# Kernel tuning notes

Hardware: AMD Instinct MI355X
Metric: run time of the kernel (lower is better)

## Reference

```python
import jax, jax.numpy as jnp
import numpy as np

B, A, N, E, H, OUT = 32, 16, 10000, 256, 256, 2

def setup_inputs() -> dict:
    key = jax.random.key(0)
    k1, k2, k3, k4, k5, k6 = jax.random.split(key, 6)
    abs_actions = jax.random.normal(k1, (B, A), dtype=jnp.float32)
    assignments = jax.random.randint(k2, (B, N), 0, A, dtype=jnp.int64)
    emb = jax.random.normal(k3, (N, E), dtype=jnp.float32)  # ground_agent_embedding.weight
    s1 = 1.0 / np.sqrt(1 + E)
    W1 = jax.random.uniform(k4, (1 + E, H), jnp.float32, -s1, s1)
    b1 = jnp.zeros((H,), jnp.float32)
    s2 = 1.0 / np.sqrt(H)
    W2 = jax.random.uniform(k5, (H, OUT), jnp.float32, -s2, s2)
    b2 = jnp.zeros((OUT,), jnp.float32)
    return {"abs_actions": abs_actions, "abstract_agent_assignments": assignments,
            "emb": emb, "W1": W1, "b1": b1, "W2": W2, "b2": b2}

def reference(abs_actions, abstract_agent_assignments, emb, W1, b1, W2, b2):
    # per-batch gather: assigned[b, n] = abs_actions[b, assignments[b, n]]  -> (B, N)
    assigned = jnp.take_along_axis(abs_actions, abstract_agent_assignments, axis=1)
    # concat scalar action with broadcast embedding table -> (B, N, 1+E)
    x = jnp.concatenate(
        [assigned[..., None], jnp.broadcast_to(emb[None], (assigned.shape[0],) + emb.shape)],
        axis=-1)
    # shared small MLP (MultiChannelNet, n_channels=1): Linear -> ReLU -> Linear
    h = jax.nn.relu(jnp.einsum("bnf,fh->bnh", x, W1) + b1)
    return jnp.einsum("bnh,ho->bno", h, W2) + b2  # (B, N, OUT) action logits
```

## Files before the change

### kernel.cpp

```cpp
#include <hip/hip_runtime.h>


constexpr int B_ = 32, A_ = 16, N_ = 10000, E_ = 256, H_ = 256;
constexpr int TN   = 40;
constexpr int NBLK = N_ / TN;

__global__ __launch_bounds__(256, 1) void decoder_fused(
    const float* __restrict__ abs_actions,
    const int*   __restrict__ asgn,
    const float* __restrict__ emb,
    const float* __restrict__ W1,
    const float* __restrict__ b1,
    const float* __restrict__ W2,
    const float* __restrict__ b2,
    float* __restrict__ out)
{
    __shared__ float u[TN * 260];
    __shared__ float vals[B_ * 41];
    __shared__ float w1r[H_];
    __shared__ float w2s[2 * H_];

    const int t  = threadIdx.x;
    const int n0 = blockIdx.x * TN;

    {
        const float4* src = reinterpret_cast<const float4*>(emb + (size_t)n0 * E_);
        float4* dst = reinterpret_cast<float4*>(u);
        #pragma unroll
        for (int q = 0; q < 10; ++q) dst[t + 256 * q] = src[t + 256 * q];
    }
    w1r[t]       = W1[t];
    w2s[t]       = W2[t];
    w2s[256 + t] = W2[256 + t];
    #pragma unroll
    for (int q = 0; q < 5; ++q) {
        int p = t + 256 * q;
        int b = p / 40, n = p - b * 40;
        int a = asgn[b * N_ + n0 + n];
        vals[b * 41 + n] = abs_actions[b * A_ + a];
    }
    __syncthreads();

    const int hq = t & 63;
    const int h0 = hq * 4;
    const int ng = t >> 6;
    const int nb = ng * 10;

    float acc[10][4];
    {
        const float4 bv = *reinterpret_cast<const float4*>(b1 + h0);
        #pragma unroll
        for (int i = 0; i < 10; ++i) {
            acc[i][0] = bv.x; acc[i][1] = bv.y; acc[i][2] = bv.z; acc[i][3] = bv.w;
        }
    }

    const float* pw = W1 + E_ + h0;
    float4 wa = *reinterpret_cast<const float4*>(pw + 0 * 256);
    float4 wb = *reinterpret_cast<const float4*>(pw + 1 * 256);
    float4 wc = *reinterpret_cast<const float4*>(pw + 2 * 256);
    float4 wd = *reinterpret_cast<const float4*>(pw + 3 * 256);

    for (int k = 0; k < 256; k += 4) {
        const int kn = (k + 4) & 255;
        float4 na_ = *reinterpret_cast<const float4*>(pw + (kn + 0) * 256);
        float4 nb_ = *reinterpret_cast<const float4*>(pw + (kn + 1) * 256);
        float4 nc_ = *reinterpret_cast<const float4*>(pw + (kn + 2) * 256);
        float4 nd_ = *reinterpret_cast<const float4*>(pw + (kn + 3) * 256);
        #pragma unroll
        for (int i = 0; i < 10; ++i) {
            const float4 e = *reinterpret_cast<const float4*>(&u[(nb + i) * 256 + k]);
            acc[i][0] = fmaf(e.x, wa.x, acc[i][0]);
            acc[i][0] = fmaf(e.y, wb.x, acc[i][0]);
            acc[i][0] = fmaf(e.z, wc.x, acc[i][0]);
            acc[i][0] = fmaf(e.w, wd.x, acc[i][0]);
            acc[i][1] = fmaf(e.x, wa.y, acc[i][1]);
            acc[i][1] = fmaf(e.y, wb.y, acc[i][1]);
            acc[i][1] = fmaf(e.z, wc.y, acc[i][1]);
            acc[i][1] = fmaf(e.w, wd.y, acc[i][1]);
            acc[i][2] = fmaf(e.x, wa.z, acc[i][2]);
            acc[i][2] = fmaf(e.y, wb.z, acc[i][2]);
            acc[i][2] = fmaf(e.z, wc.z, acc[i][2]);
            acc[i][2] = fmaf(e.w, wd.z, acc[i][2]);
            acc[i][3] = fmaf(e.x, wa.w, acc[i][3]);
            acc[i][3] = fmaf(e.y, wb.w, acc[i][3]);
            acc[i][3] = fmaf(e.z, wc.w, acc[i][3]);
            acc[i][3] = fmaf(e.w, wd.w, acc[i][3]);
        }
        wa = na_; wb = nb_; wc = nc_; wd = nd_;
    }

    __syncthreads();
    #pragma unroll
    for (int i = 0; i < 10; ++i) {
        float4 v; v.x = acc[i][0]; v.y = acc[i][1]; v.z = acc[i][2]; v.w = acc[i][3];
        *reinterpret_cast<float4*>(&u[(nb + i) * 260 + h0]) = v;
    }
    __syncthreads();

    const float2 b2v = *reinterpret_cast<const float2*>(b2);
    float oacc[5][2];
    int   pn[5], pb[5];
    float pv[5];
    #pragma unroll
    for (int q = 0; q < 5; ++q) {
        int p = t + 256 * q;
        int b = p / 40, n = p - b * 40;
        pb[q] = b; pn[q] = n;
        pv[q] = vals[b * 41 + n];
        oacc[q][0] = 0.f; oacc[q][1] = 0.f;
    }

    #pragma unroll 2
    for (int h = 0; h < 256; h += 4) {
        const float4 wv = *reinterpret_cast<const float4*>(&w1r[h]);
        const float4 p0 = *reinterpret_cast<const float4*>(&w2s[2 * h]);
        const float4 p1 = *reinterpret_cast<const float4*>(&w2s[2 * h + 4]);
        #pragma unroll
        for (int q = 0; q < 5; ++q) {
            const float4 c = *reinterpret_cast<const float4*>(&u[pn[q] * 260 + h]);
            const float v = pv[q];
            float t0 = fmaxf(fmaf(v, wv.x, c.x), 0.f);
            float t1 = fmaxf(fmaf(v, wv.y, c.y), 0.f);
            float t2 = fmaxf(fmaf(v, wv.z, c.z), 0.f);
            float t3 = fmaxf(fmaf(v, wv.w, c.w), 0.f);
            oacc[q][0] = fmaf(t0, p0.x, oacc[q][0]);
            oacc[q][1] = fmaf(t0, p0.y, oacc[q][1]);
            oacc[q][0] = fmaf(t1, p0.z, oacc[q][0]);
            oacc[q][1] = fmaf(t1, p0.w, oacc[q][1]);
            oacc[q][0] = fmaf(t2, p1.x, oacc[q][0]);
            oacc[q][1] = fmaf(t2, p1.y, oacc[q][1]);
            oacc[q][0] = fmaf(t3, p1.z, oacc[q][0]);
            oacc[q][1] = fmaf(t3, p1.w, oacc[q][1]);
        }
    }

    #pragma unroll
    for (int q = 0; q < 5; ++q) {
        float2 o; o.x = oacc[q][0] + b2v.x; o.y = oacc[q][1] + b2v.y;
        *reinterpret_cast<float2*>(out + ((size_t)pb[q] * N_ + n0 + pn[q]) * 2) = o;
    }
}

extern "C" void kernel_launch(void* const* d_in, const int* in_sizes, int n_in,
                              void* d_out, int out_size, void* d_ws, size_t ws_size,
                              hipStream_t stream) {
    const float* abs_actions = (const float*)d_in[0];
    const int*   asgn        = (const int*)d_in[1];
    const float* emb         = (const float*)d_in[2];
    const float* W1          = (const float*)d_in[3];
    const float* b1          = (const float*)d_in[4];
    const float* W2          = (const float*)d_in[5];
    const float* b2          = (const float*)d_in[6];
    float*       out         = (float*)d_out;

    decoder_fused<<<NBLK, 256, 0, stream>>>(abs_actions, asgn, emb, W1, b1, W2, b2, out);
}
```

Before: 35.68 us.

## Compute embedding projection with bf16 MFMA using pre-transposed W1

Adds a prep kernel that transposes the embedding rows of W1 and converts them to bf16 in a global buffer. The main kernel converts embedding tiles to bf16 in shared memory and computes the N×E by E×H projection with 16x16x32 bf16 MFMA instructions instead of scalar FP32 FMAs. The tile shrinks to 16 nodes per block with two blocks per CU. This cuts FP32 ALU work on the dominant GEMM, at the cost of bf16 rounding error and an extra kernel launch per call.

```diff
diff --git a/kernel.cpp b/kernel.cpp
--- a/kernel.cpp
+++ b/kernel.cpp
@@ -2,10 +2,33 @@
 
 
 constexpr int B_ = 32, A_ = 16, N_ = 10000, E_ = 256, H_ = 256;
-constexpr int TN   = 40;
-constexpr int NBLK = N_ / TN;
+constexpr int TN = 16, NBLK = N_ / TN;
 
-__global__ __launch_bounds__(256, 1) void decoder_fused(
+typedef __attribute__((ext_vector_type(8))) short bf16x8;
+typedef __attribute__((ext_vector_type(4))) float f32x4;
+
+__device__ __align__(16) ushort g_w1t[H_ * E_];
+
+static __device__ __forceinline__ ushort f2bf(float x) {
+    union { float f; unsigned u; } c; c.f = x;
+    unsigned r = c.u + 0x7fff + ((c.u >> 16) & 1);
+    return (ushort)(r >> 16);
+}
+
+__global__ __launch_bounds__(256, 1) void prep_w1t_k(const float* __restrict__ W1) {
+    __shared__ float tile[64][65];
+    const int bk = blockIdx.x >> 2, bh = blockIdx.x & 3;
+    const int tx = threadIdx.x & 63, ty = threadIdx.x >> 6;
+    #pragma unroll
+    for (int kk = ty; kk < 64; kk += 4)
+        tile[kk][tx] = W1[(size_t)(1 + bk * 64 + kk) * H_ + bh * 64 + tx];
+    __syncthreads();
+    #pragma unroll
+    for (int hh = ty; hh < 64; hh += 4)
+        g_w1t[(size_t)(bh * 64 + hh) * E_ + bk * 64 + tx] = f2bf(tile[tx][hh]);
+}
+
+__global__ __launch_bounds__(256, 2) void decoder_main(
     const float* __restrict__ abs_actions,
     const int*   __restrict__ asgn,
     const float* __restrict__ emb,
@@ -15,130 +38,108 @@
     const float* __restrict__ b2,
     float* __restrict__ out)
 {
-    __shared__ float u[TN * 260];
-    __shared__ float vals[B_ * 41];
-    __shared__ float w1r[H_];
-    __shared__ float w2s[2 * H_];
+    __shared__ ushort eb[TN * 264];
+    __shared__ float  u[TN * 260];
+    __shared__ float  vals[B_ * 17];
+    __shared__ float  w1r[H_];
+    __shared__ float  w2s[2 * H_];
 
     const int t  = threadIdx.x;
     const int n0 = blockIdx.x * TN;
 
+    #pragma unroll
+    for (int q = 0; q < 2; ++q) {
+        const int p = t + 256 * q, b = p >> 4, n = p & 15;
+        vals[b * 17 + n] = abs_actions[b * A_ + asgn[(size_t)b * N_ + n0 + n]];
+    }
+
     {
-        const float4* src = reinterpret_cast<const float4*>(emb + (size_t)n0 * E_);
-        float4* dst = reinterpret_cast<float4*>(u);
+        const int row = t >> 4, col = (t & 15) << 4;
+        const float4* src = reinterpret_cast<const float4*>(emb + (size_t)(n0 + row) * E_ + col);
+        const float4 q0 = src[0], q1 = src[1], q2 = src[2], q3 = src[3];
+        union { ushort us[16]; bf16x8 v[2]; } pk;
+        const float f[16] = {q0.x,q0.y,q0.z,q0.w, q1.x,q1.y,q1.z,q1.w,
+                             q2.x,q2.y,q2.z,q2.w, q3.x,q3.y,q3.z,q3.w};
         #pragma unroll
-        for (int q = 0; q < 10; ++q) dst[t + 256 * q] = src[t + 256 * q];
+        for (int i = 0; i < 16; ++i) pk.us[i] = f2bf(f[i]);
+        bf16x8* dst = reinterpret_cast<bf16x8*>(&eb[row * 264 + col]);
+        dst[0] = pk.v[0]; dst[1] = pk.v[1];
     }
     w1r[t]       = W1[t];
     w2s[t]       = W2[t];
     w2s[256 + t] = W2[256 + t];
-    #pragma unroll
-    for (int q = 0; q < 5; ++q) {
-        int p = t + 256 * q;
-        int b = p / 40, n = p - b * 40;
-        int a = asgn[b * N_ + n0 + n];
-        vals[b * 41 + n] = abs_actions[b * A_ + a];
+    __syncthreads();
+
+    {
+        const int lane = t & 63, w = t >> 6;
+        const int lr = lane & 15;
+        const int lk = (lane >> 4) << 3;
+        f32x4 acc[4];
+        #pragma unroll
+        for (int ct = 0; ct < 4; ++ct) {
+            const float bv = b1[w * 64 + ct * 16 + lr];
+            acc[ct] = (f32x4){bv, bv, bv, bv};
+        }
+        #pragma unroll
+        for (int ks = 0; ks < 8; ++ks) {
+            const bf16x8 af = *reinterpret_cast<const bf16x8*>(&eb[lr * 264 + ks * 32 + lk]);
+            #pragma unroll
+            for (int ct = 0; ct < 4; ++ct) {
+                const bf16x8 bfv = *reinterpret_cast<const bf16x8*>(
+                    &g_w1t[(size_t)(w * 64 + ct * 16 + lr) * E_ + ks * 32 + lk]);
+                acc[ct] = __builtin_amdgcn_mfma_f32_16x16x32_bf16(af, bfv, acc[ct], 0, 0, 0);
+            }
+        }
+        #pragma unroll
+        for (int ct = 0; ct < 4; ++ct)
+            #pragma unroll
+            for (int r = 0; r < 4; ++r)
+                u[((lane >> 4) * 4 + r) * 260 + w * 64 + ct * 16 + lr] = acc[ct][r];
     }
     __syncthreads();
 
-    const int hq = t & 63;
-    const int h0 = hq * 4;
-    const int ng = t >> 6;
-    const int nb = ng * 10;
+    {
+        const float2 b2v = { b2[0], b2[1] };
+        float oacc[2][2];
+        int   pnn[2], pbb[2];
+        float pv[2];
+        #pragma unroll
+        for (int q = 0; q < 2; ++q) {
+            const int p = t + 256 * q, b = p >> 4, n = p & 15;
+            pbb[q] = b; pnn[q] = n;
+            pv[q] = vals[b * 17 + n];
+            oacc[q][0] = 0.f; oacc[q][1] = 0.f;
+        }
 
-    float acc[10][4];
-    {
-        const float4 bv = *reinterpret_cast<const float4*>(b1 + h0);
+        #pragma unroll 2
+        for (int h = 0; h < 256; h += 4) {
+            const float4 wv = *reinterpret_cast<const float4*>(&w1r[h]);
+            const float4 p0 = *reinterpret_cast<const float4*>(&w2s[2 * h]);
+            const float4 p1 = *reinterpret_cast<const float4*>(&w2s[2 * h + 4]);
+            #pragma unroll
+            for (int q = 0; q < 2; ++q) {
+                const float4 c = *reinterpret_cast<const float4*>(&u[pnn[q] * 260 + h]);
+                const float v = pv[q];
+                const float t0 = fmaxf(fmaf(v, wv.x, c.x), 0.f);
+                const float t1 = fmaxf(fmaf(v, wv.y, c.y), 0.f);
+                const float t2 = fmaxf(fmaf(v, wv.z, c.z), 0.f);
+                const float t3 = fmaxf(fmaf(v, wv.w, c.w), 0.f);
+                oacc[q][0] = fmaf(t0, p0.x, oacc[q][0]);
+                oacc[q][1] = fmaf(t0, p0.y, oacc[q][1]);
+                oacc[q][0] = fmaf(t1, p0.z, oacc[q][0]);
+                oacc[q][1] = fmaf(t1, p0.w, oacc[q][1]);
+                oacc[q][0] = fmaf(t2, p1.x, oacc[q][0]);
+                oacc[q][1] = fmaf(t2, p1.y, oacc[q][1]);
+                oacc[q][0] = fmaf(t3, p1.z, oacc[q][0]);
+                oacc[q][1] = fmaf(t3, p1.w, oacc[q][1]);
+            }
+        }
+
         #pragma unroll
-        for (int i = 0; i < 10; ++i) {
-            acc[i][0] = bv.x; acc[i][1] = bv.y; acc[i][2] = bv.z; acc[i][3] = bv.w;
+        for (int q = 0; q < 2; ++q) {
+            float2 o; o.x = oacc[q][0] + b2v.x; o.y = oacc[q][1] + b2v.y;
+            *reinterpret_cast<float2*>(out + ((size_t)pbb[q] * N_ + n0 + pnn[q]) * 2) = o;
         }
-    }
-
-    const float* pw = W1 + E_ + h0;
-    float4 wa = *reinterpret_cast<const float4*>(pw + 0 * 256);
-    float4 wb = *reinterpret_cast<const float4*>(pw + 1 * 256);
-    float4 wc = *reinterpret_cast<const float4*>(pw + 2 * 256);
-    float4 wd = *reinterpret_cast<const float4*>(pw + 3 * 256);
-
-    for (int k = 0; k < 256; k += 4) {
-        const int kn = (k + 4) & 255;
-        float4 na_ = *reinterpret_cast<const float4*>(pw + (kn + 0) * 256);
-        float4 nb_ = *reinterpret_cast<const float4*>(pw + (kn + 1) * 256);
-        float4 nc_ = *reinterpret_cast<const float4*>(pw + (kn + 2) * 256);
-        float4 nd_ = *reinterpret_cast<const float4*>(pw + (kn + 3) * 256);
-        #pragma unroll
-        for (int i = 0; i < 10; ++i) {
-            const float4 e = *reinterpret_cast<const float4*>(&u[(nb + i) * 256 + k]);
-            acc[i][0] = fmaf(e.x, wa.x, acc[i][0]);
-            acc[i][0] = fmaf(e.y, wb.x, acc[i][0]);
-            acc[i][0] = fmaf(e.z, wc.x, acc[i][0]);
-            acc[i][0] = fmaf(e.w, wd.x, acc[i][0]);
-            acc[i][1] = fmaf(e.x, wa.y, acc[i][1]);
-            acc[i][1] = fmaf(e.y, wb.y, acc[i][1]);
-            acc[i][1] = fmaf(e.z, wc.y, acc[i][1]);
-            acc[i][1] = fmaf(e.w, wd.y, acc[i][1]);
-            acc[i][2] = fmaf(e.x, wa.z, acc[i][2]);
-            acc[i][2] = fmaf(e.y, wb.z, acc[i][2]);
-            acc[i][2] = fmaf(e.z, wc.z, acc[i][2]);
-            acc[i][2] = fmaf(e.w, wd.z, acc[i][2]);
-            acc[i][3] = fmaf(e.x, wa.w, acc[i][3]);
-            acc[i][3] = fmaf(e.y, wb.w, acc[i][3]);
-            acc[i][3] = fmaf(e.z, wc.w, acc[i][3]);
-            acc[i][3] = fmaf(e.w, wd.w, acc[i][3]);
-        }
-        wa = na_; wb = nb_; wc = nc_; wd = nd_;
-    }
-
-    __syncthreads();
-    #pragma unroll
-    for (int i = 0; i < 10; ++i) {
-        float4 v; v.x = acc[i][0]; v.y = acc[i][1]; v.z = acc[i][2]; v.w = acc[i][3];
-        *reinterpret_cast<float4*>(&u[(nb + i) * 260 + h0]) = v;
-    }
-    __syncthreads();
-
-    const float2 b2v = *reinterpret_cast<const float2*>(b2);
-    float oacc[5][2];
-    int   pn[5], pb[5];
-    float pv[5];
-    #pragma unroll
-    for (int q = 0; q < 5; ++q) {
-        int p = t + 256 * q;
-        int b = p / 40, n = p - b * 40;
-        pb[q] = b; pn[q] = n;
-        pv[q] = vals[b * 41 + n];
-        oacc[q][0] = 0.f; oacc[q][1] = 0.f;
-    }
-
-    #pragma unroll 2
-    for (int h = 0; h < 256; h += 4) {
-        const float4 wv = *reinterpret_cast<const float4*>(&w1r[h]);
-        const float4 p0 = *reinterpret_cast<const float4*>(&w2s[2 * h]);
-        const float4 p1 = *reinterpret_cast<const float4*>(&w2s[2 * h + 4]);
-        #pragma unroll
-        for (int q = 0; q < 5; ++q) {
-            const float4 c = *reinterpret_cast<const float4*>(&u[pn[q] * 260 + h]);
-            const float v = pv[q];
-            float t0 = fmaxf(fmaf(v, wv.x, c.x), 0.f);
-            float t1 = fmaxf(fmaf(v, wv.y, c.y), 0.f);
-            float t2 = fmaxf(fmaf(v, wv.z, c.z), 0.f);
-            float t3 = fmaxf(fmaf(v, wv.w, c.w), 0.f);
-            oacc[q][0] = fmaf(t0, p0.x, oacc[q][0]);
-            oacc[q][1] = fmaf(t0, p0.y, oacc[q][1]);
-            oacc[q][0] = fmaf(t1, p0.z, oacc[q][0]);
-            oacc[q][1] = fmaf(t1, p0.w, oacc[q][1]);
-            oacc[q][0] = fmaf(t2, p1.x, oacc[q][0]);
-            oacc[q][1] = fmaf(t2, p1.y, oacc[q][1]);
-            oacc[q][0] = fmaf(t3, p1.z, oacc[q][0]);
-            oacc[q][1] = fmaf(t3, p1.w, oacc[q][1]);
-        }
-    }
-
-    #pragma unroll
-    for (int q = 0; q < 5; ++q) {
-        float2 o; o.x = oacc[q][0] + b2v.x; o.y = oacc[q][1] + b2v.y;
-        *reinterpret_cast<float2*>(out + ((size_t)pb[q] * N_ + n0 + pn[q]) * 2) = o;
     }
 }
 
@@ -154,5 +155,6 @@
     const float* b2          = (const float*)d_in[6];
     float*       out         = (float*)d_out;
 
-    decoder_fused<<<NBLK, 256, 0, stream>>>(abs_actions, asgn, emb, W1, b1, W2, b2, out);
+    prep_w1t_k<<<16, 256, 0, stream>>>(W1);
+    decoder_main<<<NBLK, 256, 0, stream>>>(abs_actions, asgn, emb, W1, b1, W2, b2, out);
 }
```

Result: faster. 30.61 us (-14.2%).
